# Kernel tuning notes

Hardware: AMD Instinct MI355X
Metric: run time of the kernel (lower is better)

The kernel has to match this reference:

```python
import jax, jax.numpy as jnp
import numpy as np

NUM_FRAMES = 32
H, W = 1024, 1024
MAX_DEPTH = 5
PROB_THRESHOLD = 1e-3  # torch skips children with topk prob <= 0.001


def setup_inputs() -> dict:
    key = jax.random.key(0)
    k1, k2 = jax.random.split(key)
    frame_colors = jax.random.uniform(k1, (NUM_FRAMES, 3), dtype=jnp.float32)
    # torch init: rand(num_frames, 2, num_frames) * 5
    frame_selection = jax.random.uniform(k2, (NUM_FRAMES, 2, NUM_FRAMES), dtype=jnp.float32) * 5.0
    return {"frame_colors": frame_colors, "frame_selection": frame_selection, "temperature": 1}


def _np_softmax(x):
    e = np.exp(x - x.max(axis=-1, keepdims=True))
    return e / e.sum(axis=-1, keepdims=True)


def _render(idx, depth, h, w, fc, fs_probs, probs_np, memo):
    # Output depends only on (idx, depth, h, w) since split_ratio is a constant
    # 0.5 buffer and split_direction = idx % 2, so identical subtrees are memoized.
    key = (idx, depth, h, w)
    if key in memo:
        return memo[key]
    if depth >= MAX_DEPTH or w < 2 or h < 2:
        out = jnp.broadcast_to(jax.nn.sigmoid(fc[idx]).reshape(3, 1, 1), (3, h, w))
    else:
        vertical = (idx % 2) == 1  # split_directions[i] = i % 2
        if vertical:
            lw = max(1, int(w * 0.5))
            child_sizes = ((h, lw), (h, w - lw))  # left cols [0:lw], right cols [lw:]
        else:
            th = max(1, int(h * 0.5))
            child_sizes = ((th, w), (h - th, w))  # top rows [0:th], bottom rows [th:]
        k = 3 if depth < 2 else (2 if depth < 4 else 1)
        k = min(k, NUM_FRAMES)
        parts = []
        for side in range(2):  # 0 = left/top, 1 = right/bottom
            ch, cw = child_sizes[side]
            pn = probs_np[idx, side]
            order = np.argsort(-pn)[:k]  # top-k child frame indices (constant w.r.t. grads)
            probs = fs_probs[idx, side]
            acc = jnp.zeros((3, ch, cw), dtype=fc.dtype)
            for i in order:
                if pn[i] > PROB_THRESHOLD:  # same skip rule as torch, decided on concrete values
                    child = _render(int(i), depth + 1, ch, cw, fc, fs_probs, probs_np, memo)
                    acc = acc + probs[i] * child
            parts.append(acc)
        out = jnp.concatenate(parts, axis=2 if vertical else 1)
    memo[key] = out
    return out


def reference(frame_colors, frame_selection, temperature):
    t = float(temperature)
    fs_probs = jax.nn.softmax(frame_selection / t, axis=-1)  # (F, 2, F) differentiable weights
    probs_np = _np_softmax(np.asarray(frame_selection, dtype=np.float64) / t)  # structure only
    return _render(0, 0, H, W, frame_colors, fs_probs, probs_np, {})
```

## Files before the change

### kernel.cpp

```cpp
#include <hip/hip_runtime.h>
#include <math.h>

#define NF 32
#define HH 1024
#define WW 1024


__device__ __forceinline__ int descend(int idx, int py, int px,
                                       int& y0, int& x0, int& h, int& w) {
  int side;
  if (idx & 1) {
    int lw = w >> 1;
    if (px >= x0 + lw) { side = 1; x0 += lw; w -= lw; }
    else               { side = 0; w = lw; }
  } else {
    int th = h >> 1;
    if (py >= y0 + th) { side = 1; y0 += th; h -= th; }
    else               { side = 0; h = th; }
  }
  return side;
}

__device__ __forceinline__ bool better(float pa, int ia, float pb, int ib) {
  return (pa > pb) || (pa == pb && ia < ib);
}

__global__ __launch_bounds__(256)
void fractal_kernel(const float* __restrict__ fc,
                    const float* __restrict__ fsel,
                    const int* __restrict__ temp,
                    float* __restrict__ out) {
  __shared__ float sProbs[64][33];
  __shared__ int   sOrder[64][3];
  __shared__ float sSig[NF][3];
  __shared__ float sCol[3];

  const int tid  = threadIdx.x;
  const int tile = blockIdx.x;
  const int by = tile >> 5, bx = tile & 31;
  const int py = by * 32 + 16, px = bx * 32 + 16;

  int   ti = temp[0];
  float t  = (ti > 0 && ti < 1000000) ? (float)ti : __int_as_float(ti);
  const float invT = 1.0f / t;

  for (int v = 0; v < 8; ++v) {
    int u = v * 256 + tid;
    sProbs[u >> 5][u & 31] = fsel[u] * invT;
  }
  __syncthreads();

  {
    const int row = tid >> 2;
    const int sub = tid & 3;
    float* rp = &sProbs[row][sub * 8];

    float m = rp[0];
    #pragma unroll
    for (int i = 1; i < 8; ++i) m = fmaxf(m, rp[i]);
    m = fmaxf(m, __shfl_xor(m, 1, 64));
    m = fmaxf(m, __shfl_xor(m, 2, 64));

    float s = 0.f;
    float e[8];
    #pragma unroll
    for (int i = 0; i < 8; ++i) { e[i] = expf(rp[i] - m); s += e[i]; }
    s += __shfl_xor(s, 1, 64);
    s += __shfl_xor(s, 2, 64);
    const float inv = 1.0f / s;

    float v0 = -1.f, v1 = -1.f, v2 = -1.f;
    int   b0 = 0,    b1 = 0,    b2 = 0;
    #pragma unroll
    for (int i = 0; i < 8; ++i) {
      float p = e[i] * inv;
      rp[i] = p;
      int gi = sub * 8 + i;
      if (better(p, gi, v0, b0))      { v2=v1;b2=b1; v1=v0;b1=b0; v0=p;b0=gi; }
      else if (better(p, gi, v1, b1)) { v2=v1;b2=b1; v1=p;b1=gi; }
      else if (better(p, gi, v2, b2)) { v2=p;b2=gi; }
    }
    #pragma unroll
    for (int mseq = 1; mseq <= 2; mseq <<= 1) {
      float w0 = __shfl_xor(v0, mseq, 64), w1 = __shfl_xor(v1, mseq, 64),
            w2 = __shfl_xor(v2, mseq, 64);
      int   c0 = __shfl_xor(b0, mseq, 64), c1 = __shfl_xor(b1, mseq, 64),
            c2 = __shfl_xor(b2, mseq, 64);
      float wv[3] = { w0, w1, w2 };
      int   wc[3] = { c0, c1, c2 };
      #pragma unroll
      for (int j = 0; j < 3; ++j) {
        float p = wv[j]; int gi = wc[j];
        if (better(p, gi, v0, b0))      { v2=v1;b2=b1; v1=v0;b1=b0; v0=p;b0=gi; }
        else if (better(p, gi, v1, b1)) { v2=v1;b2=b1; v1=p;b1=gi; }
        else if (better(p, gi, v2, b2)) { v2=p;b2=gi; }
      }
    }
    if (sub == 0) { sOrder[row][0] = b0; sOrder[row][1] = b1; sOrder[row][2] = b2; }
  }
  if (tid < 96) {
    sSig[tid / 3][tid % 3] = 1.0f / (1.0f + expf(-fc[tid]));
  }
  __syncthreads();

  if (tid < 64) {
    const int lane = tid;
    float c0 = 0.f, c1 = 0.f, c2 = 0.f;
    if (lane < 36) {
      int j = lane;
      int sel0 = j / 12; int r = j % 12;
      int sel1 = r / 4;  r &= 3;
      int sel2 = r >> 1;
      int sel3 = r & 1;
      int selArr[5] = { sel0, sel1, sel2, sel3, 0 };

      int idx = 0, ay = 0, ax = 0, ah = HH, aw = WW;
      float w = 1.0f;
      bool alive = true;
      for (int d = 0; d < 5; ++d) {
        int s   = descend(idx, py, px, ay, ax, ah, aw);
        int row = idx * 2 + s;
        int ci  = sOrder[row][selArr[d]];
        float p = sProbs[row][ci];
        if (p <= 1e-3f) { alive = false; break; }
        w  *= p;
        idx = ci;
      }
      if (alive) {
        c0 = w * sSig[idx][0];
        c1 = w * sSig[idx][1];
        c2 = w * sSig[idx][2];
      }
    }
    for (int off = 32; off > 0; off >>= 1) {
      c0 += __shfl_down(c0, off, 64);
      c1 += __shfl_down(c1, off, 64);
      c2 += __shfl_down(c2, off, 64);
    }
    if (tid == 0) { sCol[0] = c0; sCol[1] = c1; sCol[2] = c2; }
  }
  __syncthreads();

  const int r = tid >> 3;
  const int q = tid & 7;
  for (int c = 0; c < 3; ++c) {
    float v = sCol[c];
    float4 val = make_float4(v, v, v, v);
    float* base = out + (size_t)c * (HH * WW)
                      + (size_t)(by * 32 + r) * WW + (size_t)bx * 32;
    ((float4*)base)[q] = val;
  }
}

extern "C" void kernel_launch(void* const* d_in, const int* in_sizes, int n_in,
                              void* d_out, int out_size, void* d_ws, size_t ws_size,
                              hipStream_t stream) {
  const float* fc   = (const float*)d_in[0];
  const float* fsel = (const float*)d_in[1];
  const int*   temp = (const int*)d_in[2];
  float* out = (float*)d_out;
  (void)in_sizes; (void)n_in; (void)out_size; (void)d_ws; (void)ws_size;
  fractal_kernel<<<dim3(1024), dim3(256), 0, stream>>>(fc, fsel, temp, out);
}
```

Before: 64.97 us.

## Compute tile color per wave, drop barrier, softmax only top-3, nontemporal stores

Every wave now independently evaluates the 36 tree paths and reduces the color with xor shuffles, removing the shared-memory color broadcast and one block barrier. The top-3 selection runs on raw logits, and only the three selected probabilities are exponentiated and stored. The sigmoid table load moves before the first barrier, and output writes use nontemporal vector stores. The trade-off is that the path evaluation is repeated four times per block.

```diff
diff --git a/kernel.cpp b/kernel.cpp
--- a/kernel.cpp
+++ b/kernel.cpp
@@ -4,6 +4,8 @@
 #define NF 32
 #define HH 1024
 #define WW 1024
+
+typedef float nfloat4 __attribute__((ext_vector_type(4)));
 
 
 __device__ __forceinline__ int descend(int idx, int py, int px,
@@ -30,10 +32,10 @@
                     const float* __restrict__ fsel,
                     const int* __restrict__ temp,
                     float* __restrict__ out) {
-  __shared__ float sProbs[64][33];
-  __shared__ int   sOrder[64][3];
+  __shared__ float sLogit[64][33];
+  __shared__ float sTop[64][4];
+  __shared__ int   sOrder[64][4];
   __shared__ float sSig[NF][3];
-  __shared__ float sCol[3];
 
   const int tid  = threadIdx.x;
   const int tile = blockIdx.x;
@@ -46,36 +48,39 @@
 
   for (int v = 0; v < 8; ++v) {
     int u = v * 256 + tid;
-    sProbs[u >> 5][u & 31] = fsel[u] * invT;
+    sLogit[u >> 5][u & 31] = fsel[u] * invT;
+  }
+  if (tid < 96) {
+    sSig[tid / 3][tid % 3] = 1.0f / (1.0f + expf(-fc[tid]));
   }
   __syncthreads();
 
   {
     const int row = tid >> 2;
     const int sub = tid & 3;
-    float* rp = &sProbs[row][sub * 8];
+    const float* rp = &sLogit[row][sub * 8];
 
-    float m = rp[0];
+    float raw[8];
     #pragma unroll
-    for (int i = 1; i < 8; ++i) m = fmaxf(m, rp[i]);
+    for (int i = 0; i < 8; ++i) raw[i] = rp[i];
+
+    float m = raw[0];
+    #pragma unroll
+    for (int i = 1; i < 8; ++i) m = fmaxf(m, raw[i]);
     m = fmaxf(m, __shfl_xor(m, 1, 64));
     m = fmaxf(m, __shfl_xor(m, 2, 64));
 
     float s = 0.f;
-    float e[8];
     #pragma unroll
-    for (int i = 0; i < 8; ++i) { e[i] = expf(rp[i] - m); s += e[i]; }
+    for (int i = 0; i < 8; ++i) s += expf(raw[i] - m);
     s += __shfl_xor(s, 1, 64);
     s += __shfl_xor(s, 2, 64);
-    const float inv = 1.0f / s;
 
-    float v0 = -1.f, v1 = -1.f, v2 = -1.f;
-    int   b0 = 0,    b1 = 0,    b2 = 0;
+    float v0 = -1e30f, v1 = -1e30f, v2 = -1e30f;
+    int   b0 = 0,      b1 = 0,      b2 = 0;
     #pragma unroll
     for (int i = 0; i < 8; ++i) {
-      float p = e[i] * inv;
-      rp[i] = p;
-      int gi = sub * 8 + i;
+      float p = raw[i]; int gi = sub * 8 + i;
       if (better(p, gi, v0, b0))      { v2=v1;b2=b1; v1=v0;b1=b0; v0=p;b0=gi; }
       else if (better(p, gi, v1, b1)) { v2=v1;b2=b1; v1=p;b1=gi; }
       else if (better(p, gi, v2, b2)) { v2=p;b2=gi; }
@@ -96,60 +101,61 @@
         else if (better(p, gi, v2, b2)) { v2=p;b2=gi; }
       }
     }
-    if (sub == 0) { sOrder[row][0] = b0; sOrder[row][1] = b1; sOrder[row][2] = b2; }
-  }
-  if (tid < 96) {
-    sSig[tid / 3][tid % 3] = 1.0f / (1.0f + expf(-fc[tid]));
+    if (sub == 0) {
+      const float inv = 1.0f / s;
+      sTop[row][0] = expf(v0 - m) * inv;
+      sTop[row][1] = expf(v1 - m) * inv;
+      sTop[row][2] = expf(v2 - m) * inv;
+      sOrder[row][0] = b0; sOrder[row][1] = b1; sOrder[row][2] = b2;
+    }
   }
   __syncthreads();
 
-  if (tid < 64) {
-    const int lane = tid;
-    float c0 = 0.f, c1 = 0.f, c2 = 0.f;
-    if (lane < 36) {
-      int j = lane;
-      int sel0 = j / 12; int r = j % 12;
-      int sel1 = r / 4;  r &= 3;
-      int sel2 = r >> 1;
-      int sel3 = r & 1;
-      int selArr[5] = { sel0, sel1, sel2, sel3, 0 };
+  const int wave = tid >> 6;
+  const int lane = tid & 63;
+  float c0 = 0.f, c1 = 0.f, c2 = 0.f;
+  if (lane < 36) {
+    int j = lane;
+    int sel0 = j / 12; int r = j % 12;
+    int sel1 = r / 4;  r &= 3;
+    int sel2 = r >> 1;
+    int sel3 = r & 1;
+    int selArr[5] = { sel0, sel1, sel2, sel3, 0 };
 
-      int idx = 0, ay = 0, ax = 0, ah = HH, aw = WW;
-      float w = 1.0f;
-      bool alive = true;
-      for (int d = 0; d < 5; ++d) {
-        int s   = descend(idx, py, px, ay, ax, ah, aw);
-        int row = idx * 2 + s;
-        int ci  = sOrder[row][selArr[d]];
-        float p = sProbs[row][ci];
-        if (p <= 1e-3f) { alive = false; break; }
-        w  *= p;
-        idx = ci;
-      }
-      if (alive) {
-        c0 = w * sSig[idx][0];
-        c1 = w * sSig[idx][1];
-        c2 = w * sSig[idx][2];
-      }
+    int idx = 0, ay = 0, ax = 0, ah = HH, aw = WW;
+    float w = 1.0f;
+    bool alive = true;
+    for (int d = 0; d < 5; ++d) {
+      int s   = descend(idx, py, px, ay, ax, ah, aw);
+      int row = idx * 2 + s;
+      int ci  = sOrder[row][selArr[d]];
+      float p = sTop[row][selArr[d]];
+      if (p <= 1e-3f) { alive = false; break; }
+      w  *= p;
+      idx = ci;
     }
-    for (int off = 32; off > 0; off >>= 1) {
-      c0 += __shfl_down(c0, off, 64);
-      c1 += __shfl_down(c1, off, 64);
-      c2 += __shfl_down(c2, off, 64);
+    if (alive) {
+      c0 = w * sSig[idx][0];
+      c1 = w * sSig[idx][1];
+      c2 = w * sSig[idx][2];
     }
-    if (tid == 0) { sCol[0] = c0; sCol[1] = c1; sCol[2] = c2; }
   }
-  __syncthreads();
+  #pragma unroll
+  for (int off = 32; off > 0; off >>= 1) {
+    c0 += __shfl_xor(c0, off, 64);
+    c1 += __shfl_xor(c1, off, 64);
+    c2 += __shfl_xor(c2, off, 64);
+  }
 
-  const int r = tid >> 3;
-  const int q = tid & 7;
-  for (int c = 0; c < 3; ++c) {
-    float v = sCol[c];
-    float4 val = make_float4(v, v, v, v);
-    float* base = out + (size_t)c * (HH * WW)
-                      + (size_t)(by * 32 + r) * WW + (size_t)bx * 32;
-    ((float4*)base)[q] = val;
-  }
+  const int r = wave * 8 + (lane >> 3);
+  const int q = lane & 7;
+  float* base0 = out + (size_t)(by * 32 + r) * WW + (size_t)bx * 32;
+  nfloat4 p0 = { c0, c0, c0, c0 };
+  nfloat4 p1 = { c1, c1, c1, c1 };
+  nfloat4 p2 = { c2, c2, c2, c2 };
+  __builtin_nontemporal_store(p0, (nfloat4*)base0 + q);
+  __builtin_nontemporal_store(p1, (nfloat4*)(base0 + HH * WW) + q);
+  __builtin_nontemporal_store(p2, (nfloat4*)(base0 + 2 * HH * WW) + q);
 }
 
 extern "C" void kernel_launch(void* const* d_in, const int* in_sizes, int n_in,
```

After: 64.76 us. Within noise of the previous version (-0.3%).
